# Kernel optimization log

Measured on AMD Instinct MI355X. Metric: run time of the kernel, lower is better.

The kernel has to match this reference:

```python
import jax, jax.numpy as jnp
import numpy as np

NUM_GRAPHS = 64
NUM_LAYERS = 3
HEADS = 4
HID = 64
DMODEL = HEADS * HID  # 256
NUM_EDGE_TYPES = 8
NUM_CLASSES = 2
N_NODES = 30000
N_EDGES = 240000


def setup_inputs() -> dict:
    key = jax.random.key(0)
    ks = jax.random.split(key, 16)
    s = 0.05
    x = jax.random.normal(ks[0], (N_NODES, DMODEL), jnp.float32)
    edge_index = jax.random.randint(ks[1], (2, N_EDGES), 0, N_NODES)
    batch = jnp.sort(jax.random.randint(ks[2], (N_NODES,), 0, NUM_GRAPHS))
    edge_type_ids = jax.random.randint(ks[3], (N_EDGES,), 0, NUM_EDGE_TYPES)
    # stacked per-layer conv params (all layers are DMODEL -> HEADS*HID = DMODEL)
    Wq = jax.random.normal(ks[4], (NUM_LAYERS, DMODEL, DMODEL), jnp.float32) * s
    bq = jax.random.normal(ks[5], (NUM_LAYERS, DMODEL), jnp.float32) * s
    Wk = jax.random.normal(ks[6], (NUM_LAYERS, DMODEL, DMODEL), jnp.float32) * s
    bk = jax.random.normal(ks[7], (NUM_LAYERS, DMODEL), jnp.float32) * s
    Wv = jax.random.normal(ks[8], (NUM_LAYERS, DMODEL, DMODEL), jnp.float32) * s
    bv = jax.random.normal(ks[9], (NUM_LAYERS, DMODEL), jnp.float32) * s
    Eemb = jax.random.normal(ks[10], (NUM_LAYERS, NUM_EDGE_TYPES, DMODEL), jnp.float32) * s
    # 1-layer GRU (PyTorch layout: [3*hid, in], gate order r, z, n)
    W_ih = jax.random.normal(ks[11], (3 * HID, DMODEL), jnp.float32) * s
    b_ih = jax.random.normal(ks[12], (3 * HID,), jnp.float32) * s
    W_hh = jax.random.normal(ks[13], (3 * HID, HID), jnp.float32) * s
    b_hh = jax.random.normal(ks[14], (3 * HID,), jnp.float32) * s
    W_fc = jax.random.normal(ks[15], (NUM_CLASSES, HID), jnp.float32) * s
    b_fc = jnp.zeros((NUM_CLASSES,), jnp.float32)
    return dict(x=x, edge_index=edge_index, batch=batch, edge_type_ids=edge_type_ids,
                Wq=Wq, bq=bq, Wk=Wk, bk=bk, Wv=Wv, bv=bv, Eemb=Eemb,
                W_ih=W_ih, b_ih=b_ih, W_hh=W_hh, b_hh=b_hh, W_fc=W_fc, b_fc=b_fc)


def reference(x, edge_index, batch, edge_type_ids, Wq, bq, Wk, bk, Wv, bv, Eemb,
              W_ih, b_ih, W_hh, b_hh, W_fc, b_fc):
    N = x.shape[0]
    src, dst = edge_index[0], edge_index[1]  # messages flow src -> dst
    scale = 1.0 / jnp.sqrt(jnp.float32(HID))
    for l in range(NUM_LAYERS):
        q = (x @ Wq[l] + bq[l]).reshape(N, HEADS, HID)
        k_all = x @ Wk[l] + bk[l]  # [N, DMODEL]
        v_all = x @ Wv[l] + bv[l]
        ete = Eemb[l][edge_type_ids]  # edge-type conditioning, [E, DMODEL]
        k = (k_all[src] + ete).reshape(-1, HEADS, HID)
        v = (v_all[src] + ete).reshape(-1, HEADS, HID)
        scores = jnp.einsum('ehd,ehd->eh', q[dst], k) * scale  # [E, H]
        # per-destination-node segment softmax (stable)
        m = jax.ops.segment_max(scores, dst, num_segments=N)
        ex = jnp.exp(scores - m[dst])
        den = jax.ops.segment_sum(ex, dst, num_segments=N)
        alpha = ex / (den[dst] + 1e-16)
        agg = jax.ops.segment_sum(alpha[..., None] * v, dst, num_segments=N)
        x = jax.nn.elu(agg.reshape(N, DMODEL))
    # global mean pool over graphs
    cnt = jax.ops.segment_sum(jnp.ones((N,), x.dtype), batch, num_segments=NUM_GRAPHS)
    g = jax.ops.segment_sum(x, batch, num_segments=NUM_GRAPHS) / jnp.maximum(cnt, 1.0)[:, None]
    # single GRU step from h0 = 0 (seq_len == 1)
    h0 = jnp.zeros((NUM_GRAPHS, HID), x.dtype)
    gi = g @ W_ih.T + b_ih
    gh = h0 @ W_hh.T + b_hh
    ir, iz, inn = jnp.split(gi, 3, axis=-1)
    hr, hz, hn = jnp.split(gh, 3, axis=-1)
    r = jax.nn.sigmoid(ir + hr)
    z = jax.nn.sigmoid(iz + hz)
    n = jnp.tanh(inn + r * hn)
    h = (1.0 - z) * n + z * h0
    return h @ W_fc.T + b_fc  # [NUM_GRAPHS, NUM_CLASSES]
```

## Files before the change

### kernel.cpp

```cpp
#include <hip/hip_runtime.h>
#include <math.h>

#define N_NODES 30000
#define N_EDGES 240000
#define DMODEL 256
#define NETYPES 8
#define NGRAPHS 64
#define NLAYERS 3

typedef __attribute__((ext_vector_type(8))) short short8;
typedef __attribute__((ext_vector_type(4))) float f32x4;

__device__ __forceinline__ unsigned short f2bf(float f) {
  union { float f; unsigned u; } v; v.f = f;
  unsigned r = v.u + 0x7FFF + ((v.u >> 16) & 1);
  return (unsigned short)(r >> 16);
}
__device__ __forceinline__ float bf2f(unsigned short h) {
  union { unsigned u; float f; } v; v.u = ((unsigned)h) << 16;
  return v.f;
}

__device__ __forceinline__ void async_g2l(const unsigned short* g, unsigned short* l) {
  __builtin_amdgcn_global_load_lds(
      (const __attribute__((address_space(1))) void*)g,
      (__attribute__((address_space(3))) void*)l, 16, 0, 0);
}

__global__ void k_count_deg(const int* __restrict__ dst, int* __restrict__ deg) {
  int e = blockIdx.x * blockDim.x + threadIdx.x;
  if (e < N_EDGES) atomicAdd(&deg[dst[e]], 1);
}

__global__ __launch_bounds__(1024) void k_scan(const int* __restrict__ deg,
                                               int* __restrict__ rowstart,
                                               int* __restrict__ cursor) {
  const int C = 30;
  int tid = threadIdx.x;
  int base = tid * C;
  int vals[C];
  int sum = 0;
#pragma unroll
  for (int j = 0; j < C; ++j) {
    int idx = base + j;
    int v = (idx < N_NODES) ? deg[idx] : 0;
    vals[j] = sum;
    sum += v;
  }
  int lane = tid & 63, wv = tid >> 6;
  int s = sum;
#pragma unroll
  for (int off = 1; off < 64; off <<= 1) {
    int t2 = __shfl_up(s, off);
    if (lane >= off) s += t2;
  }
  __shared__ int wsum[16];
  if (lane == 63) wsum[wv] = s;
  __syncthreads();
  if (tid == 0) {
    int a = 0;
#pragma unroll
    for (int i = 0; i < 16; ++i) { int t2 = wsum[i]; wsum[i] = a; a += t2; }
    rowstart[N_NODES] = a;
  }
  __syncthreads();
  int texcl = wsum[wv] + (s - sum);
#pragma unroll
  for (int j = 0; j < C; ++j) {
    int idx = base + j;
    if (idx < N_NODES) {
      int p = texcl + vals[j];
      rowstart[idx] = p;
      cursor[idx]   = p;
    }
  }
}

__global__ void k_scatter(const int* __restrict__ src, const int* __restrict__ dst,
                          const int* __restrict__ etype, int* __restrict__ cursor,
                          int* __restrict__ packed) {
  int e = blockIdx.x * blockDim.x + threadIdx.x;
  if (e < N_EDGES) {
    int p = atomicAdd(&cursor[dst[e]], 1);
    packed[p] = src[e] * NETYPES + etype[e];
  }
}

__global__ __launch_bounds__(256) void k_cvt_w(
    const float* __restrict__ Wq, const float* __restrict__ Wk, const float* __restrict__ Wv,
    unsigned short* __restrict__ wthi) {
  __shared__ float tile[32][33];
  int k0 = blockIdx.x * 32;
  int n0g = blockIdx.y * 32;
  int l = blockIdx.z;
  int which = n0g >> 8;
  int col0 = n0g & 255;
  const float* W = (which == 0) ? Wq : ((which == 1) ? Wk : Wv);
  int c = threadIdx.x & 31, r = threadIdx.x >> 5;
#pragma unroll
  for (int rr = 0; rr < 4; ++rr) {
    int kk = r + rr * 8;
    tile[kk][c] = W[(size_t)l * 65536 + (size_t)(k0 + kk) * 256 + col0 + c];
  }
  __syncthreads();
  int kk = threadIdx.x & 31, nn0 = threadIdx.x >> 5;
#pragma unroll
  for (int rr = 0; rr < 4; ++rr) {
    int nn = nn0 + rr * 8;
    wthi[((size_t)l * 768 + n0g + nn) * 256 + k0 + kk] = f2bf(tile[kk][nn]);
  }
}

__global__ void k_cvt_b(const float* __restrict__ bq, const float* __restrict__ bk,
                        const float* __restrict__ bv, float* __restrict__ bcat) {
  int idx = blockIdx.x * 256 + threadIdx.x;
  if (idx >= NLAYERS * 768) return;
  int n = idx % 768, l = idx / 768;
  int which = n >> 8, col = n & 255;
  const float* b = (which == 0) ? bq : ((which == 1) ? bk : bv);
  bcat[idx] = b[l * 256 + col];
}

__global__ void k_cvt_x(const float* __restrict__ x, unsigned short* __restrict__ xhi,
                        unsigned short* __restrict__ xlo) {
  int i = blockIdx.x * 256 + threadIdx.x;
  if (i < N_NODES * 256) {
    float v = x[i];
    unsigned short h = f2bf(v);
    xhi[i] = h;
    xlo[i] = f2bf(v - bf2f(h));
  }
}

__global__ __launch_bounds__(256) void k_gemm_mfma(
    const unsigned short* __restrict__ Ahi, const unsigned short* __restrict__ Alo,
    const unsigned short* __restrict__ Bhi,
    const float* __restrict__ bcat, float* __restrict__ qbuf,
    unsigned short* __restrict__ kv) {
  __shared__ unsigned short smem[3 * 4096];
  unsigned short* sAhi = smem;
  unsigned short* sAlo = smem + 4096;
  unsigned short* sBhi = smem + 8192;

  int tid = threadIdx.x;
  int lane = tid & 63, wave = tid >> 6;
  int bx = blockIdx.x;
  int row0 = (bx / 6) * 128;
  int n0 = (bx % 6) * 128;
  int wm = (wave >> 1) * 64, wn = (wave & 1) * 64;
  int quad = lane >> 4, l16 = lane & 15;
  int chunk = lane & 3;
  int srow = wave * 32 + (lane >> 2);

  f32x4 acc[4][4];
#pragma unroll
  for (int i = 0; i < 4; ++i)
#pragma unroll
    for (int j = 0; j < 4; ++j) acc[i][j] = (f32x4)(0.f);

  for (int k0 = 0; k0 < 256; k0 += 32) {
#pragma unroll
    for (int j = 0; j < 2; ++j) {
      int r = srow + j * 16;
      int ldsoff = wave * 1024 + j * 512;
      int garA = row0 + r; if (garA >= N_NODES) garA = N_NODES - 1;
      size_t aoff = (size_t)garA * 256 + k0 + chunk * 8;
      async_g2l(Ahi + aoff, sAhi + ldsoff);
      async_g2l(Alo + aoff, sAlo + ldsoff);
      size_t boff = (size_t)(n0 + r) * 256 + k0 + chunk * 8;
      async_g2l(Bhi + boff, sBhi + ldsoff);
    }
    __syncthreads();
    short8 ah[4], al[4], bh[4];
#pragma unroll
    for (int i = 0; i < 4; ++i) {
      int off = (wm + i * 16 + l16) * 32 + quad * 8;
      ah[i] = *(const short8*)(sAhi + off);
      al[i] = *(const short8*)(sAlo + off);
    }
#pragma unroll
    for (int j = 0; j < 4; ++j) {
      int off = (wn + j * 16 + l16) * 32 + quad * 8;
      bh[j] = *(const short8*)(sBhi + off);
    }
#pragma unroll
    for (int i = 0; i < 4; ++i)
#pragma unroll
      for (int j = 0; j < 4; ++j) {
        acc[i][j] = __builtin_amdgcn_mfma_f32_16x16x32_bf16(ah[i], bh[j], acc[i][j], 0, 0, 0);
        acc[i][j] = __builtin_amdgcn_mfma_f32_16x16x32_bf16(al[i], bh[j], acc[i][j], 0, 0, 0);
      }
    __syncthreads();
  }

  float bj[4];
#pragma unroll
  for (int j = 0; j < 4; ++j) bj[j] = bcat[n0 + wn + j * 16 + l16];
  bool isq = (n0 < 256);
#pragma unroll
  for (int i = 0; i < 4; ++i) {
    int rowb = row0 + wm + i * 16 + quad * 4;
#pragma unroll
    for (int r = 0; r < 4; ++r) {
      int grow = rowb + r;
      if (grow < N_NODES) {
        if (isq) {
          float* cp = qbuf + (size_t)grow * 256 + n0 + wn + l16;
#pragma unroll
          for (int j = 0; j < 4; ++j) cp[j * 16] = acc[i][j][r] + bj[j];
        } else {
          unsigned short* cp = kv + (size_t)grow * 512 + (n0 - 256) + wn + l16;
#pragma unroll
          for (int j = 0; j < 4; ++j) cp[j * 16] = f2bf(acc[i][j][r] + bj[j]);
        }
      }
    }
  }
}

__global__ __launch_bounds__(256) void k_attn(
    const float* __restrict__ qbuf, const unsigned short* __restrict__ kv,
    const int* __restrict__ rowstart, const int* __restrict__ packed,
    const float* __restrict__ Eemb_l,
    unsigned short* __restrict__ xhi, unsigned short* __restrict__ xlo) {
  __shared__ float ete_s[NETYPES * 256];
  int t = threadIdx.x;
#pragma unroll
  for (int i = 0; i < NETYPES; ++i) ete_s[i * 256 + t] = Eemb_l[i * 256 + t];
  __syncthreads();
  int lane = t & 63;
  int n = blockIdx.x * 4 + (t >> 6);
  float4 q4 = ((const float4*)(qbuf + (size_t)n * 256))[lane];
  int rs = rowstart[n], re = rowstart[n + 1];
  float l1 = 0.f, ax1 = 0.f, ay1 = 0.f, az1 = 0.f, aw1 = 0.f;
  float l2 = 0.f, ax2 = 0.f, ay2 = 0.f, az2 = 0.f, aw2 = 0.f;
  int i = rs;
  for (; i + 2 <= re; i += 2) {
    int pkA = packed[i], pkB = packed[i + 1];
    const unsigned short* baseA = kv + (size_t)(pkA >> 3) * 512;
    const unsigned short* baseB = kv + (size_t)(pkB >> 3) * 512;
    ushort4 kA = ((const ushort4*)baseA)[lane];
    ushort4 vA = ((const ushort4*)(baseA + 256))[lane];
    ushort4 kB = ((const ushort4*)baseB)[lane];
    ushort4 vB = ((const ushort4*)(baseB + 256))[lane];
    float4 eA = ((const float4*)(ete_s + (pkA & 7) * 256))[lane];
    float4 eB = ((const float4*)(ete_s + (pkB & 7) * 256))[lane];
    float pA = (bf2f(kA.x) + eA.x) * q4.x + (bf2f(kA.y) + eA.y) * q4.y +
               (bf2f(kA.z) + eA.z) * q4.z + (bf2f(kA.w) + eA.w) * q4.w;
    float pB = (bf2f(kB.x) + eB.x) * q4.x + (bf2f(kB.y) + eB.y) * q4.y +
               (bf2f(kB.z) + eB.z) * q4.z + (bf2f(kB.w) + eB.w) * q4.w;
    pA += __shfl_xor(pA, 1); pB += __shfl_xor(pB, 1);
    pA += __shfl_xor(pA, 2); pB += __shfl_xor(pB, 2);
    pA += __shfl_xor(pA, 4); pB += __shfl_xor(pB, 4);
    pA += __shfl_xor(pA, 8); pB += __shfl_xor(pB, 8);
    float e1 = __expf(pA * 0.125f);
    float e2 = __expf(pB * 0.125f);
    l1 += e1; l2 += e2;
    ax1 = fmaf(e1, bf2f(vA.x) + eA.x, ax1);
    ay1 = fmaf(e1, bf2f(vA.y) + eA.y, ay1);
    az1 = fmaf(e1, bf2f(vA.z) + eA.z, az1);
    aw1 = fmaf(e1, bf2f(vA.w) + eA.w, aw1);
    ax2 = fmaf(e2, bf2f(vB.x) + eB.x, ax2);
    ay2 = fmaf(e2, bf2f(vB.y) + eB.y, ay2);
    az2 = fmaf(e2, bf2f(vB.z) + eB.z, az2);
    aw2 = fmaf(e2, bf2f(vB.w) + eB.w, aw2);
  }
  if (i < re) {
    int pk = packed[i];
    const unsigned short* base = kv + (size_t)(pk >> 3) * 512;
    ushort4 kh = ((const ushort4*)base)[lane];
    ushort4 vh = ((const ushort4*)(base + 256))[lane];
    float4 e4 = ((const float4*)(ete_s + (pk & 7) * 256))[lane];
    float p = (bf2f(kh.x) + e4.x) * q4.x + (bf2f(kh.y) + e4.y) * q4.y +
              (bf2f(kh.z) + e4.z) * q4.z + (bf2f(kh.w) + e4.w) * q4.w;
    p += __shfl_xor(p, 1);
    p += __shfl_xor(p, 2);
    p += __shfl_xor(p, 4);
    p += __shfl_xor(p, 8);
    float e1 = __expf(p * 0.125f);
    l1 += e1;
    ax1 = fmaf(e1, bf2f(vh.x) + e4.x, ax1);
    ay1 = fmaf(e1, bf2f(vh.y) + e4.y, ay1);
    az1 = fmaf(e1, bf2f(vh.z) + e4.z, az1);
    aw1 = fmaf(e1, bf2f(vh.w) + e4.w, aw1);
  }
  float l = l1 + l2;
  float inv = 1.f / (l + 1e-16f);
  float4 o;
  o.x = (ax1 + ax2) * inv; o.y = (ay1 + ay2) * inv;
  o.z = (az1 + az2) * inv; o.w = (aw1 + aw2) * inv;
  o.x = o.x > 0.f ? o.x : expm1f(o.x);
  o.y = o.y > 0.f ? o.y : expm1f(o.y);
  o.z = o.z > 0.f ? o.z : expm1f(o.z);
  o.w = o.w > 0.f ? o.w : expm1f(o.w);
  unsigned short h0 = f2bf(o.x), h1 = f2bf(o.y), h2 = f2bf(o.z), h3 = f2bf(o.w);
  ushort4 hv, lv;
  hv.x = h0; hv.y = h1; hv.z = h2; hv.w = h3;
  lv.x = f2bf(o.x - bf2f(h0)); lv.y = f2bf(o.y - bf2f(h1));
  lv.z = f2bf(o.z - bf2f(h2)); lv.w = f2bf(o.w - bf2f(h3));
  size_t base_o = (size_t)n * 256 + lane * 4;
  *(ushort4*)(xhi + base_o) = hv;
  *(ushort4*)(xlo + base_o) = lv;
}

__global__ __launch_bounds__(256) void k_pool_partial(
    const unsigned short* __restrict__ xhi, const unsigned short* __restrict__ xlo,
    const int* __restrict__ batch, float* __restrict__ gacc) {
  int t = threadIdx.x;
  int base = blockIdx.x * 128;
  int end = base + 128; if (end > N_NODES) end = N_NODES;
  __shared__ int bsh[128];
  if (t < 128 && base + t < N_NODES) bsh[t] = batch[base + t];
  __syncthreads();
  float acc = 0.f;
  int cur = bsh[0];
  for (int n = base; n < end; ++n) {
    int g = bsh[n - base];
    if (g != cur) {
      atomicAdd(&gacc[cur * 256 + t], acc);
      acc = 0.f; cur = g;
    }
    size_t idx = (size_t)n * 256 + t;
    acc += bf2f(xhi[idx]) + bf2f(xlo[idx]);
  }
  atomicAdd(&gacc[cur * 256 + t], acc);
}

__device__ inline int lower_bound_dev(const int* a, int n, int val) {
  int lo = 0, hi = n;
  while (lo < hi) {
    int mid = (lo + hi) >> 1;
    if (a[mid] < val) lo = mid + 1; else hi = mid;
  }
  return lo;
}

__global__ __launch_bounds__(256) void k_gru_fc(
    const float* __restrict__ gacc, const int* __restrict__ batch,
    const float* __restrict__ W_ih, const float* __restrict__ b_ih,
    const float* __restrict__ b_hh, const float* __restrict__ W_fc,
    const float* __restrict__ b_fc, float* __restrict__ out) {
  __shared__ float gv[256];
  __shared__ float gates[192];
  __shared__ float h[64];
  int gr = blockIdx.x, t = threadIdx.x;
  int s0 = lower_bound_dev(batch, N_NODES, gr);
  int e0 = lower_bound_dev(batch, N_NODES, gr + 1);
  float c = (e0 > s0) ? (float)(e0 - s0) : 1.f;
  gv[t] = gacc[gr * 256 + t] / c;
  __syncthreads();
  if (t < 192) {
    const float* wr = W_ih + t * 256;
    float s = b_ih[t];
    for (int k = 0; k < 256; ++k) s = fmaf(gv[k], wr[k], s);
    gates[t] = s;
  }
  __syncthreads();
  if (t < 64) {
    float r  = 1.f / (1.f + expf(-(gates[t] + b_hh[t])));
    float z  = 1.f / (1.f + expf(-(gates[64 + t] + b_hh[64 + t])));
    float nn = tanhf(gates[128 + t] + r * b_hh[128 + t]);
    h[t] = (1.f - z) * nn;
  }
  __syncthreads();
  if (t < 2) {
    const float* wr = W_fc + t * 64;
    float s = b_fc[t];
    for (int k = 0; k < 64; ++k) s = fmaf(h[k], wr[k], s);
    out[gr * 2 + t] = s;
  }
}

extern "C" void kernel_launch(void* const* d_in, const int* in_sizes, int n_in,
                              void* d_out, int out_size, void* d_ws, size_t ws_size,
                              hipStream_t stream) {
  const float* x     = (const float*)d_in[0];
  const int* edge_index = (const int*)d_in[1];
  const int* batch   = (const int*)d_in[2];
  const int* etype   = (const int*)d_in[3];
  const float* Wq    = (const float*)d_in[4];
  const float* bq    = (const float*)d_in[5];
  const float* Wk    = (const float*)d_in[6];
  const float* bk    = (const float*)d_in[7];
  const float* Wv    = (const float*)d_in[8];
  const float* bv    = (const float*)d_in[9];
  const float* Eemb  = (const float*)d_in[10];
  const float* W_ih  = (const float*)d_in[11];
  const float* b_ih  = (const float*)d_in[12];
  const float* b_hh  = (const float*)d_in[14];
  const float* W_fc  = (const float*)d_in[15];
  const float* b_fc  = (const float*)d_in[16];
  float* out = (float*)d_out;

  const int* src = edge_index;
  const int* dst = edge_index + N_EDGES;

  float* qbuf  = (float*)d_ws;
  float* gacc  = qbuf + (size_t)N_NODES * 256;
  float* bcat  = gacc + NGRAPHS * 256;
  unsigned short* kv   = (unsigned short*)(bcat + NLAYERS * 768);
  unsigned short* xhi  = kv + (size_t)N_NODES * 512;
  unsigned short* xlo  = xhi + (size_t)N_NODES * 256;
  unsigned short* wthi = xlo + (size_t)N_NODES * 256;
  int* deg      = (int*)(wthi + (size_t)NLAYERS * 768 * 256);
  int* rowstart = deg + N_NODES;
  int* cursor   = rowstart + N_NODES + 1;
  int* packed   = cursor + N_NODES;

  hipMemsetAsync(deg, 0, N_NODES * sizeof(int), stream);
  hipMemsetAsync(gacc, 0, NGRAPHS * 256 * sizeof(float), stream);
  k_count_deg<<<(N_EDGES + 255) / 256, 256, 0, stream>>>(dst, deg);
  k_scan<<<1, 1024, 0, stream>>>(deg, rowstart, cursor);
  k_scatter<<<(N_EDGES + 255) / 256, 256, 0, stream>>>(src, dst, etype, cursor, packed);

  k_cvt_w<<<dim3(8, 24, 3), 256, 0, stream>>>(Wq, Wk, Wv, wthi);
  k_cvt_b<<<(NLAYERS * 768 + 255) / 256, 256, 0, stream>>>(bq, bk, bv, bcat);
  k_cvt_x<<<(N_NODES * 256 + 255) / 256, 256, 0, stream>>>(x, xhi, xlo);

  for (int l = 0; l < NLAYERS; ++l) {
    k_gemm_mfma<<<235 * 6, 256, 0, stream>>>(
        xhi, xlo, wthi + (size_t)l * 768 * 256,
        bcat + l * 768, qbuf, kv);
    k_attn<<<N_NODES / 4, 256, 0, stream>>>(qbuf, kv, rowstart, packed,
                                            Eemb + (size_t)l * NETYPES * 256, xhi, xlo);
  }
  k_pool_partial<<<(N_NODES + 127) / 128, 256, 0, stream>>>(xhi, xlo, batch, gacc);
  k_gru_fc<<<NGRAPHS, 256, 0, stream>>>(gacc, batch, W_ih, b_ih, b_hh, W_fc, b_fc, out);
}
```

Measured before the change: 510.7 us.

## Interleave K/V per node, precompute edge-type score terms, and swizzle GEMM blocks

The GEMM epilogue now writes K and V interleaved per feature, so the attention kernel fetches both with a single 16-byte gather per edge. The edge-type embedding is moved out of the per-edge loop: q·Eemb is precomputed per node, head and type into a small shared table. The value-side embedding contribution is accumulated as per-type attention weights and applied once after the loop. The edge loop is unrolled by four to keep more gathers in flight, and GEMM blocks are remapped into groups of eight row tiles for better L2 reuse. In exchange, the GEMM stores become strided 2-byte writes, and the extra per-node table setup costs a second barrier.

```diff
diff --git a/kernel.cpp b/kernel.cpp
--- a/kernel.cpp
+++ b/kernel.cpp
@@ -9,6 +9,7 @@
 #define NLAYERS 3
 
 typedef __attribute__((ext_vector_type(8))) short short8;
+typedef __attribute__((ext_vector_type(8))) unsigned short ushort8;
 typedef __attribute__((ext_vector_type(4))) float f32x4;
 
 __device__ __forceinline__ unsigned short f2bf(float f) {
@@ -136,17 +137,21 @@
     const unsigned short* __restrict__ Ahi, const unsigned short* __restrict__ Alo,
     const unsigned short* __restrict__ Bhi,
     const float* __restrict__ bcat, float* __restrict__ qbuf,
-    unsigned short* __restrict__ kv) {
+    unsigned short* __restrict__ kvb) {
   __shared__ unsigned short smem[3 * 4096];
   unsigned short* sAhi = smem;
   unsigned short* sAlo = smem + 4096;
   unsigned short* sBhi = smem + 8192;
 
+  int x = blockIdx.x & 7, j0 = blockIdx.x >> 3;
+  int rg = j0 / 6, c0 = j0 % 6;
+  int r0 = rg * 8 + x;
+  if (r0 >= 235) return;
+  int row0 = r0 * 128;
+  int n0 = c0 * 128;
+
   int tid = threadIdx.x;
   int lane = tid & 63, wave = tid >> 6;
-  int bx = blockIdx.x;
-  int row0 = (bx / 6) * 128;
-  int n0 = (bx % 6) * 128;
   int wm = (wave >> 1) * 64, wn = (wave & 1) * 64;
   int quad = lane >> 4, l16 = lane & 15;
   int chunk = lane & 3;
@@ -196,7 +201,6 @@
   float bj[4];
 #pragma unroll
   for (int j = 0; j < 4; ++j) bj[j] = bcat[n0 + wn + j * 16 + l16];
-  bool isq = (n0 < 256);
 #pragma unroll
   for (int i = 0; i < 4; ++i) {
     int rowb = row0 + wm + i * 16 + quad * 4;
@@ -204,91 +208,99 @@
     for (int r = 0; r < 4; ++r) {
       int grow = rowb + r;
       if (grow < N_NODES) {
-        if (isq) {
-          float* cp = qbuf + (size_t)grow * 256 + n0 + wn + l16;
-#pragma unroll
-          for (int j = 0; j < 4; ++j) cp[j * 16] = acc[i][j][r] + bj[j];
-        } else {
-          unsigned short* cp = kv + (size_t)grow * 512 + (n0 - 256) + wn + l16;
-#pragma unroll
-          for (int j = 0; j < 4; ++j) cp[j * 16] = f2bf(acc[i][j][r] + bj[j]);
+#pragma unroll
+        for (int j = 0; j < 4; ++j) {
+          int col = n0 + wn + l16 + j * 16;
+          float val = acc[i][j][r] + bj[j];
+          if (col < 256) {
+            qbuf[(size_t)grow * 256 + col] = val;
+          } else if (col < 512) {
+            kvb[(size_t)grow * 512 + (col - 256) * 2] = f2bf(val);
+          } else {
+            kvb[(size_t)grow * 512 + (col - 512) * 2 + 1] = f2bf(val);
+          }
         }
       }
     }
   }
 }
 
+#define EDGE_BODY(PK, R8, LS, AX, AY, AZ, AW, WACC)                          \
+  {                                                                          \
+    float kx = bf2f(R8[0]), vx = bf2f(R8[1]);                                \
+    float ky = bf2f(R8[2]), vy = bf2f(R8[3]);                                \
+    float kz = bf2f(R8[4]), vz = bf2f(R8[5]);                                \
+    float kw = bf2f(R8[6]), vw = bf2f(R8[7]);                                \
+    float p = kx * q4.x + ky * q4.y + kz * q4.z + kw * q4.w;                 \
+    p += __shfl_xor(p, 1); p += __shfl_xor(p, 2);                            \
+    p += __shfl_xor(p, 4); p += __shfl_xor(p, 8);                            \
+    int et = (PK) & 7;                                                       \
+    float sc = fmaf(p, 0.125f, eqtab[eqbase + et]);                          \
+    float e1 = __expf(sc);                                                   \
+    LS += e1;                                                                \
+    WACC += ((lane & 7) == et) ? e1 : 0.f;                                   \
+    AX = fmaf(e1, vx, AX); AY = fmaf(e1, vy, AY);                            \
+    AZ = fmaf(e1, vz, AZ); AW = fmaf(e1, vw, AW);                            \
+  }
+
 __global__ __launch_bounds__(256) void k_attn(
-    const float* __restrict__ qbuf, const unsigned short* __restrict__ kv,
+    const float* __restrict__ qbuf, const unsigned short* __restrict__ kvb,
     const int* __restrict__ rowstart, const int* __restrict__ packed,
     const float* __restrict__ Eemb_l,
     unsigned short* __restrict__ xhi, unsigned short* __restrict__ xlo) {
   __shared__ float ete_s[NETYPES * 256];
+  __shared__ float eqtab[4 * 4 * 8];
   int t = threadIdx.x;
 #pragma unroll
   for (int i = 0; i < NETYPES; ++i) ete_s[i * 256 + t] = Eemb_l[i * 256 + t];
   __syncthreads();
-  int lane = t & 63;
-  int n = blockIdx.x * 4 + (t >> 6);
+  int lane = t & 63, slot = t >> 6;
+  int n = blockIdx.x * 4 + slot;
   float4 q4 = ((const float4*)(qbuf + (size_t)n * 256))[lane];
+  int head = lane >> 4;
+#pragma unroll
+  for (int ty = 0; ty < NETYPES; ++ty) {
+    float4 e4 = ((const float4*)(ete_s + ty * 256))[lane];
+    float d = e4.x * q4.x + e4.y * q4.y + e4.z * q4.z + e4.w * q4.w;
+    d += __shfl_xor(d, 1); d += __shfl_xor(d, 2);
+    d += __shfl_xor(d, 4); d += __shfl_xor(d, 8);
+    if ((lane & 15) == ty) eqtab[slot * 32 + head * 8 + ty] = d * 0.125f;
+  }
+  __syncthreads();
+  int eqbase = slot * 32 + head * 8;
   int rs = rowstart[n], re = rowstart[n + 1];
-  float l1 = 0.f, ax1 = 0.f, ay1 = 0.f, az1 = 0.f, aw1 = 0.f;
-  float l2 = 0.f, ax2 = 0.f, ay2 = 0.f, az2 = 0.f, aw2 = 0.f;
+  float l1 = 0.f, ax1 = 0.f, ay1 = 0.f, az1 = 0.f, aw1 = 0.f, w1 = 0.f;
+  float l2 = 0.f, ax2 = 0.f, ay2 = 0.f, az2 = 0.f, aw2 = 0.f, w2 = 0.f;
   int i = rs;
-  for (; i + 2 <= re; i += 2) {
-    int pkA = packed[i], pkB = packed[i + 1];
-    const unsigned short* baseA = kv + (size_t)(pkA >> 3) * 512;
-    const unsigned short* baseB = kv + (size_t)(pkB >> 3) * 512;
-    ushort4 kA = ((const ushort4*)baseA)[lane];
-    ushort4 vA = ((const ushort4*)(baseA + 256))[lane];
-    ushort4 kB = ((const ushort4*)baseB)[lane];
-    ushort4 vB = ((const ushort4*)(baseB + 256))[lane];
-    float4 eA = ((const float4*)(ete_s + (pkA & 7) * 256))[lane];
-    float4 eB = ((const float4*)(ete_s + (pkB & 7) * 256))[lane];
-    float pA = (bf2f(kA.x) + eA.x) * q4.x + (bf2f(kA.y) + eA.y) * q4.y +
-               (bf2f(kA.z) + eA.z) * q4.z + (bf2f(kA.w) + eA.w) * q4.w;
-    float pB = (bf2f(kB.x) + eB.x) * q4.x + (bf2f(kB.y) + eB.y) * q4.y +
-               (bf2f(kB.z) + eB.z) * q4.z + (bf2f(kB.w) + eB.w) * q4.w;
-    pA += __shfl_xor(pA, 1); pB += __shfl_xor(pB, 1);
-    pA += __shfl_xor(pA, 2); pB += __shfl_xor(pB, 2);
-    pA += __shfl_xor(pA, 4); pB += __shfl_xor(pB, 4);
-    pA += __shfl_xor(pA, 8); pB += __shfl_xor(pB, 8);
-    float e1 = __expf(pA * 0.125f);
-    float e2 = __expf(pB * 0.125f);
-    l1 += e1; l2 += e2;
-    ax1 = fmaf(e1, bf2f(vA.x) + eA.x, ax1);
-    ay1 = fmaf(e1, bf2f(vA.y) + eA.y, ay1);
-    az1 = fmaf(e1, bf2f(vA.z) + eA.z, az1);
-    aw1 = fmaf(e1, bf2f(vA.w) + eA.w, aw1);
-    ax2 = fmaf(e2, bf2f(vB.x) + eB.x, ax2);
-    ay2 = fmaf(e2, bf2f(vB.y) + eB.y, ay2);
-    az2 = fmaf(e2, bf2f(vB.z) + eB.z, az2);
-    aw2 = fmaf(e2, bf2f(vB.w) + eB.w, aw2);
-  }
-  if (i < re) {
-    int pk = packed[i];
-    const unsigned short* base = kv + (size_t)(pk >> 3) * 512;
-    ushort4 kh = ((const ushort4*)base)[lane];
-    ushort4 vh = ((const ushort4*)(base + 256))[lane];
-    float4 e4 = ((const float4*)(ete_s + (pk & 7) * 256))[lane];
-    float p = (bf2f(kh.x) + e4.x) * q4.x + (bf2f(kh.y) + e4.y) * q4.y +
-              (bf2f(kh.z) + e4.z) * q4.z + (bf2f(kh.w) + e4.w) * q4.w;
-    p += __shfl_xor(p, 1);
-    p += __shfl_xor(p, 2);
-    p += __shfl_xor(p, 4);
-    p += __shfl_xor(p, 8);
-    float e1 = __expf(p * 0.125f);
-    l1 += e1;
-    ax1 = fmaf(e1, bf2f(vh.x) + e4.x, ax1);
-    ay1 = fmaf(e1, bf2f(vh.y) + e4.y, ay1);
-    az1 = fmaf(e1, bf2f(vh.z) + e4.z, az1);
-    aw1 = fmaf(e1, bf2f(vh.w) + e4.w, aw1);
+  for (; i + 4 <= re; i += 4) {
+    int p0 = packed[i], p1 = packed[i + 1], p2 = packed[i + 2], p3 = packed[i + 3];
+    ushort8 r0 = *(const ushort8*)(kvb + (size_t)(p0 >> 3) * 512 + lane * 8);
+    ushort8 r1 = *(const ushort8*)(kvb + (size_t)(p1 >> 3) * 512 + lane * 8);
+    ushort8 r2 = *(const ushort8*)(kvb + (size_t)(p2 >> 3) * 512 + lane * 8);
+    ushort8 r3 = *(const ushort8*)(kvb + (size_t)(p3 >> 3) * 512 + lane * 8);
+    EDGE_BODY(p0, r0, l1, ax1, ay1, az1, aw1, w1);
+    EDGE_BODY(p1, r1, l2, ax2, ay2, az2, aw2, w2);
+    EDGE_BODY(p2, r2, l1, ax1, ay1, az1, aw1, w1);
+    EDGE_BODY(p3, r3, l2, ax2, ay2, az2, aw2, w2);
+  }
+  for (; i < re; ++i) {
+    int p0 = packed[i];
+    ushort8 r0 = *(const ushort8*)(kvb + (size_t)(p0 >> 3) * 512 + lane * 8);
+    EDGE_BODY(p0, r0, l1, ax1, ay1, az1, aw1, w1);
   }
   float l = l1 + l2;
+  float ax = ax1 + ax2, ay = ay1 + ay2, az = az1 + az2, aw = aw1 + aw2;
+  float w = w1 + w2;
+#pragma unroll
+  for (int ty = 0; ty < NETYPES; ++ty) {
+    float wt = __shfl(w, (lane & 48) + ty);
+    const float* ep = ete_s + ty * 256 + lane * 4;
+    ax = fmaf(wt, ep[0], ax); ay = fmaf(wt, ep[1], ay);
+    az = fmaf(wt, ep[2], az); aw = fmaf(wt, ep[3], aw);
+  }
   float inv = 1.f / (l + 1e-16f);
   float4 o;
-  o.x = (ax1 + ax2) * inv; o.y = (ay1 + ay2) * inv;
-  o.z = (az1 + az2) * inv; o.w = (aw1 + aw2) * inv;
+  o.x = ax * inv; o.y = ay * inv; o.z = az * inv; o.w = aw * inv;
   o.x = o.x > 0.f ? o.x : expm1f(o.x);
   o.y = o.y > 0.f ? o.y : expm1f(o.y);
   o.z = o.z > 0.f ? o.z : expm1f(o.z);
@@ -398,8 +410,8 @@
   float* qbuf  = (float*)d_ws;
   float* gacc  = qbuf + (size_t)N_NODES * 256;
   float* bcat  = gacc + NGRAPHS * 256;
-  unsigned short* kv   = (unsigned short*)(bcat + NLAYERS * 768);
-  unsigned short* xhi  = kv + (size_t)N_NODES * 512;
+  unsigned short* kvb  = (unsigned short*)(bcat + NLAYERS * 768);
+  unsigned short* xhi  = kvb + (size_t)N_NODES * 512;
   unsigned short* xlo  = xhi + (size_t)N_NODES * 256;
   unsigned short* wthi = xlo + (size_t)N_NODES * 256;
   int* deg      = (int*)(wthi + (size_t)NLAYERS * 768 * 256);
@@ -418,10 +430,10 @@
   k_cvt_x<<<(N_NODES * 256 + 255) / 256, 256, 0, stream>>>(x, xhi, xlo);
 
   for (int l = 0; l < NLAYERS; ++l) {
-    k_gemm_mfma<<<235 * 6, 256, 0, stream>>>(
+    k_gemm_mfma<<<1440, 256, 0, stream>>>(
         xhi, xlo, wthi + (size_t)l * 768 * 256,
-        bcat + l * 768, qbuf, kv);
-    k_attn<<<N_NODES / 4, 256, 0, stream>>>(qbuf, kv, rowstart, packed,
+        bcat + l * 768, qbuf, kvb);
+    k_attn<<<N_NODES / 4, 256, 0, stream>>>(qbuf, kvb, rowstart, packed,
                                             Eemb + (size_t)l * NETYPES * 256, xhi, xlo);
   }
   k_pool_partial<<<(N_NODES + 127) / 128, 256, 0, stream>>>(xhi, xlo, batch, gacc);
```

After: 530.0 us. +3.8%, slower.
